# Optimization experiments

Hardware: AMD Instinct MI355X
Metric: run time of the kernel (lower is better)

Reference implementation:

```python
import jax, jax.numpy as jnp
import numpy as np


def _he_scale(k, shape, fan_in):
    return jax.random.normal(k, shape, dtype=jnp.float32) * np.sqrt(2.0 / fan_in).astype(np.float32)


def setup_inputs() -> dict:
    key = jax.random.key(0)
    kx, kt, kp, kg, kf = jax.random.split(key, 5)
    B, H, W, C, D = 4, 64, 64, 256, 128
    x = jax.random.normal(kx, (B, H, W, C), dtype=jnp.float32)
    Wt = _he_scale(kt, (C, D), C)
    Wp = _he_scale(kp, (C, D), C)
    Wg = _he_scale(kg, (C, D), C)
    Wf = _he_scale(kf, (D, C), D)
    return {"x": x, "Wt": Wt, "Wp": Wp, "Wg": Wg, "Wf": Wf}


def _maxpool1d(z, pool_size=2, stride=1):
    # Keras MaxPool1D, padding='valid': output length = (N - pool_size)//stride + 1
    return jax.lax.reduce_window(
        z, -jnp.inf, jax.lax.max,
        window_dimensions=(1, pool_size, 1),
        window_strides=(1, stride, 1),
        padding='VALID')


def reference(x, Wt, Wp, Wg, Wf):
    B, H, W, C = x.shape
    D = Wt.shape[1]
    N = H * W
    # 1x1 conv projections == per-position matmuls
    theta = jnp.einsum('bhwc,cd->bhwd', x, Wt).reshape(B, N, D)   # [B,N,D]
    phi = jnp.einsum('bhwc,cd->bhwd', x, Wp).reshape(B, N, D)     # [B,N,D]
    g = jnp.einsum('bhwc,cd->bhwd', x, Wg).reshape(B, N, D)       # [B,N,D]
    # embedded mode: subsample phi and g (pool_size=2, strides=1) -> M = N-1
    phi = _maxpool1d(phi)                                          # [B,M,D]
    g = _maxpool1d(g)                                              # [B,M,D]
    # f = theta @ phi^T, softmax over keys (no scaling in embedded mode)
    f = jax.nn.softmax(jnp.einsum('bnd,bmd->bnm', theta, phi), axis=-1)  # [B,N,M]
    y = jnp.einsum('bnm,bmd->bnd', f, g).reshape(B, H, W, D)       # [B,H,W,D]
    # final 1x1 conv back to C channels + residual
    z = x + jnp.einsum('bhwd,dc->bhwc', y, Wf)
    return z
```

## Files before the change

kernel.cpp:

```cpp
#include <hip/hip_runtime.h>

#define B_  4
#define N_  4096
#define C_  256
#define D_  128
#define M_  4095
#define BN_ (B_ * N_)
#define KSPLIT 4

typedef _Float16 half_t;
typedef __attribute__((ext_vector_type(8))) _Float16 half8;
typedef __attribute__((ext_vector_type(4))) _Float16 half4;
typedef __attribute__((ext_vector_type(4))) float f32x4;

#define MFMA16x16x32(A, B, C) __builtin_amdgcn_mfma_f32_16x16x32_f16(A, B, C, 0, 0, 0)
#define LOG2E 1.44269504088896f

__global__ __launch_bounds__(256) void prep_kernel(
    const float* __restrict__ Wt, const float* __restrict__ Wp,
    const float* __restrict__ Wg, const float* __restrict__ Wf,
    half_t* __restrict__ WT_hi, half_t* __restrict__ WfT)
{
    const int idx = blockIdx.x * 256 + threadIdx.x;
    const int wsel = blockIdx.y;
    if (wsel < 3) {
        const float* __restrict__ W = (wsel == 0) ? Wt : (wsel == 1) ? Wp : Wg;
        const int d = idx >> 8, c = idx & 255;
        WT_hi[(size_t)wsel * 32768 + idx] = (half_t)W[(size_t)c * D_ + d];
    } else {
        const int c = idx >> 7, d = idx & 127;
        WfT[idx] = (half_t)Wf[(size_t)d * C_ + c];
    }
}

__global__ __launch_bounds__(256) void proj_kernel(
    const float* __restrict__ x, const half_t* __restrict__ WT_hi,
    half_t* __restrict__ theta, half_t* __restrict__ pphi,
    half_t* __restrict__ pgT)
{
    const int tid = threadIdx.x;
    const int lane = tid & 63;
    const int w = tid >> 6;
    const int lm = lane & 15;
    const int lq = lane >> 4;
    const int r0 = blockIdx.x * 64;
    const int which = blockIdx.y;
    const half_t* __restrict__ Wg_ = WT_hi + (size_t)which * 32768;

    __shared__ __align__(16) unsigned char lds_raw[18432];
    half_t (*Xh)[40]  = (half_t (*)[40])(lds_raw);
    half_t (*Whl)[40] = (half_t (*)[40])(lds_raw + 5120);

    f32x4 acc[8];
#pragma unroll
    for (int nb = 0; nb < 8; ++nb)
#pragma unroll
        for (int r = 0; r < 4; ++r) acc[nb][r] = 0.f;

    const int xr = tid >> 2, xc = (tid & 3) * 8;
    const int wr = tid >> 1, wc = (tid & 1) * 16;

    for (int kc = 0; kc < 8; ++kc) {
        __syncthreads();
        {
            const float* xs = x + (size_t)(r0 + xr) * C_ + kc * 32 + xc;
            float4 v0 = *(const float4*)&xs[0], v1 = *(const float4*)&xs[4];
            half8 hi;
            hi[0] = (half_t)v0.x; hi[1] = (half_t)v0.y;
            hi[2] = (half_t)v0.z; hi[3] = (half_t)v0.w;
            hi[4] = (half_t)v1.x; hi[5] = (half_t)v1.y;
            hi[6] = (half_t)v1.z; hi[7] = (half_t)v1.w;
            *(half8*)&Xh[xr][xc] = hi;
            const half_t* wsrc = Wg_ + (size_t)wr * 256 + kc * 32 + wc;
            *(half8*)&Whl[wr][wc]     = *(const half8*)&wsrc[0];
            *(half8*)&Whl[wr][wc + 8] = *(const half8*)&wsrc[8];
        }
        __syncthreads();

        half8 ah = *(const half8*)&Xh[w * 16 + lm][lq * 8];
#pragma unroll
        for (int nb = 0; nb < 8; ++nb) {
            half8 bh = *(const half8*)&Whl[nb * 16 + lm][lq * 8];
            acc[nb] = MFMA16x16x32(ah, bh, acc[nb]);
        }
    }

    if (which == 0) {
#pragma unroll
        for (int nb = 0; nb < 8; ++nb)
#pragma unroll
            for (int r = 0; r < 4; ++r)
                theta[(size_t)(r0 + w * 16 + lq * 4 + r) * D_ + nb * 16 + lm] =
                    (half_t)(acc[nb][r] * LOG2E);
        return;
    }

    __syncthreads();
    half_t (*LsT)[72] = (half_t (*)[72])(lds_raw);
#pragma unroll
    for (int nb = 0; nb < 8; ++nb) {
        const int d = nb * 16 + lm;
        const int m = w * 16 + lq * 4;
        half4 pk;
#pragma unroll
        for (int r = 0; r < 4; ++r) pk[r] = (half_t)acc[nb][r];
        *(half4*)&LsT[d][m] = pk;
    }
    if (tid < 128) {
        int rh = r0 + 64;
        if ((rh & (N_ - 1)) == 0) rh = r0 + 63;
        const float* xrow = x + (size_t)rh * C_;
        const half_t* wrow = Wg_ + (size_t)tid * 256;
        float s = 0.f;
#pragma unroll
        for (int c8 = 0; c8 < 32; ++c8) {
            half8 h = *(const half8*)&wrow[c8 * 8];
            float4 xa = *(const float4*)&xrow[c8 * 8];
            float4 xb = *(const float4*)&xrow[c8 * 8 + 4];
            s += xa.x * (float)h[0] + xa.y * (float)h[1]
               + xa.z * (float)h[2] + xa.w * (float)h[3]
               + xb.x * (float)h[4] + xb.y * (float)h[5]
               + xb.z * (float)h[6] + xb.w * (float)h[7];
        }
        LsT[tid][64] = (half_t)s;
    }
    __syncthreads();

    if (which == 1) {
        const int m = tid >> 2, dh = (tid & 3) * 32;
        half8 o[4];
#pragma unroll
        for (int j = 0; j < 32; ++j) {
            float v0 = (float)LsT[dh + j][m];
            float v1 = (float)LsT[dh + j][m + 1];
            o[j >> 3][j & 7] = (half_t)fmaxf(v0, v1);
        }
        half8* dst = (half8*)&pphi[(size_t)(r0 + m) * D_ + dh];
#pragma unroll
        for (int j = 0; j < 4; ++j) dst[j] = o[j];
    } else {
        const int d = tid >> 1, mh = (tid & 1) * 32;
        const int b = r0 / N_, m0 = r0 & (N_ - 1);
        half8 in[4];
#pragma unroll
        for (int j = 0; j < 4; ++j) in[j] = *(const half8*)&LsT[d][mh + j * 8];
        const half_t ext = LsT[d][mh + 32];
        half8 o[4];
#pragma unroll
        for (int j = 0; j < 32; ++j) {
            float v0 = (float)in[j >> 3][j & 7];
            float v1 = (j == 31) ? (float)ext : (float)in[(j + 1) >> 3][(j + 1) & 7];
            o[j >> 3][j & 7] = (half_t)fmaxf(v0, v1);
        }
        half8* dst = (half8*)&pgT[((size_t)b * D_ + d) * N_ + m0 + mh];
#pragma unroll
        for (int j = 0; j < 4; ++j) dst[j] = o[j];
    }
}

__global__ __launch_bounds__(256, 2) void attn_kernel(
    const half_t* __restrict__ theta, const half_t* __restrict__ pphi,
    const half_t* __restrict__ pgT, half_t* __restrict__ ypart,
    float* __restrict__ mstat, float* __restrict__ lstat)
{
    const int tid = threadIdx.x;
    const int lane = tid & 63;
    const int w = tid >> 6;
    const int lm = lane & 15;
    const int lq = lane >> 4;
    const int qt = blockIdx.x, ksb = blockIdx.y, b = blockIdx.z;
    const int q0 = qt * 128;
    const int kt0 = ksb * 16, kt1 = kt0 + 16;

    __shared__ half_t Ks[64][136];
    __shared__ half_t Gts[128][72];
    __shared__ half_t Ps[128][72];

    half8 qh[2][4];
#pragma unroll
    for (int nb = 0; nb < 2; ++nb) {
        const half_t* tr_ = theta + ((size_t)b * N_ + q0 + w * 32 + nb * 16 + lm) * D_;
#pragma unroll
        for (int k4 = 0; k4 < 4; ++k4)
            qh[nb][k4] = *(const half8*)(tr_ + k4 * 32 + lq * 8);
    }

    float m_i[2] = {-1e30f, -1e30f};
    float l_i[2] = {0.f, 0.f};
    f32x4 yacc[2][8];
#pragma unroll
    for (int mb = 0; mb < 2; ++mb)
#pragma unroll
        for (int dn = 0; dn < 8; ++dn)
#pragma unroll
            for (int r = 0; r < 4; ++r) yacc[mb][dn][r] = 0.f;

    for (int kt = kt0; kt < kt1; ++kt) {
        const int k0 = kt * 64;
        __syncthreads();
        {
            const int key = tid >> 2, ch = (tid & 3);
            const float4* src = (const float4*)(pphi +
                ((size_t)b * N_ + k0 + key) * D_ + ch * 32);
            float4 a0 = src[0], a1 = src[1], a2 = src[2], a3 = src[3];
            float4* dst = (float4*)&Ks[key][ch * 32];
            dst[0] = a0; dst[1] = a1; dst[2] = a2; dst[3] = a3;
            const int d = tid >> 1, kh = (tid & 1);
            const float4* gs = (const float4*)(pgT +
                ((size_t)b * D_ + d) * N_ + k0 + kh * 32);
            float4 g0 = gs[0], g1 = gs[1], g2 = gs[2], g3 = gs[3];
            float4* gd = (float4*)&Gts[d][kh * 32];
            gd[0] = g0; gd[1] = g1; gd[2] = g2; gd[3] = g3;
        }
        __syncthreads();

        f32x4 sc[4][2];
#pragma unroll
        for (int kb = 0; kb < 4; ++kb)
#pragma unroll
            for (int nb = 0; nb < 2; ++nb)
#pragma unroll
                for (int r = 0; r < 4; ++r) sc[kb][nb][r] = 0.f;
#pragma unroll
        for (int kb = 0; kb < 4; ++kb) {
#pragma unroll
            for (int k4 = 0; k4 < 4; ++k4) {
                half8 kf = *(const half8*)&Ks[kb * 16 + lm][k4 * 32 + lq * 8];
#pragma unroll
                for (int nb = 0; nb < 2; ++nb)
                    sc[kb][nb] = MFMA16x16x32(kf, qh[nb][k4], sc[kb][nb]);
            }
        }
        if (k0 + 64 > M_) {
#pragma unroll
            for (int kb = 0; kb < 4; ++kb)
#pragma unroll
                for (int r = 0; r < 4; ++r)
                    if (k0 + kb * 16 + lq * 4 + r >= M_) {
                        sc[kb][0][r] = -1e30f; sc[kb][1][r] = -1e30f;
                    }
        }
        float alpha[2];
#pragma unroll
        for (int nb = 0; nb < 2; ++nb) {
            float mt = -1e30f;
#pragma unroll
            for (int kb = 0; kb < 4; ++kb)
#pragma unroll
                for (int r = 0; r < 4; ++r) mt = fmaxf(mt, sc[kb][nb][r]);
            mt = fmaxf(mt, __shfl_xor(mt, 16, 64));
            mt = fmaxf(mt, __shfl_xor(mt, 32, 64));
            const float mnew = fmaxf(m_i[nb], mt);
            alpha[nb] = exp2f(m_i[nb] - mnew);
            m_i[nb] = mnew;
            float rs = 0.f;
#pragma unroll
            for (int kb = 0; kb < 4; ++kb)
#pragma unroll
                for (int r = 0; r < 4; ++r) {
                    float p = exp2f(sc[kb][nb][r] - mnew);
                    sc[kb][nb][r] = p;
                    rs += p;
                }
            l_i[nb] = l_i[nb] * alpha[nb] + rs;
#pragma unroll
            for (int kb = 0; kb < 4; ++kb) {
                half4 pk;
#pragma unroll
                for (int r = 0; r < 4; ++r) pk[r] = (half_t)sc[kb][nb][r];
                *(half4*)&Ps[w * 32 + nb * 16 + lm][kb * 16 + lq * 4] = pk;
            }
        }
        float alpha_t[2][4];
#pragma unroll
        for (int mb = 0; mb < 2; ++mb)
#pragma unroll
            for (int r = 0; r < 4; ++r)
                alpha_t[mb][r] = __shfl(alpha[mb], lq * 4 + r, 16);
#pragma unroll
        for (int mb = 0; mb < 2; ++mb)
#pragma unroll
            for (int dn = 0; dn < 8; ++dn)
#pragma unroll
                for (int r = 0; r < 4; ++r) yacc[mb][dn][r] *= alpha_t[mb][r];
        half8 pf[2][2];
#pragma unroll
        for (int mb = 0; mb < 2; ++mb)
#pragma unroll
            for (int k2 = 0; k2 < 2; ++k2)
                pf[mb][k2] = *(const half8*)&Ps[w * 32 + mb * 16 + lm][k2 * 32 + lq * 8];
#pragma unroll
        for (int dn = 0; dn < 8; ++dn) {
#pragma unroll
            for (int k2 = 0; k2 < 2; ++k2) {
                half8 gf = *(const half8*)&Gts[dn * 16 + lm][k2 * 32 + lq * 8];
                yacc[0][dn] = MFMA16x16x32(pf[0][k2], gf, yacc[0][dn]);
                yacc[1][dn] = MFMA16x16x32(pf[1][k2], gf, yacc[1][dn]);
            }
        }
    }

#pragma unroll
    for (int nb = 0; nb < 2; ++nb) {
        l_i[nb] += __shfl_xor(l_i[nb], 16, 64);
        l_i[nb] += __shfl_xor(l_i[nb], 32, 64);
    }
    half_t* yp = ypart + ((size_t)ksb * BN_ + (size_t)b * N_) * D_;
#pragma unroll
    for (int mb = 0; mb < 2; ++mb)
#pragma unroll
        for (int dn = 0; dn < 8; ++dn)
#pragma unroll
            for (int r = 0; r < 4; ++r)
                yp[(size_t)(q0 + w * 32 + mb * 16 + lq * 4 + r) * D_ + dn * 16 + lm] =
                    (half_t)yacc[mb][dn][r];
    if (lq == 0) {
#pragma unroll
        for (int nb = 0; nb < 2; ++nb) {
            const int row = q0 + w * 32 + nb * 16 + lm;
            mstat[(size_t)ksb * BN_ + (size_t)b * N_ + row] = m_i[nb];
            lstat[(size_t)ksb * BN_ + (size_t)b * N_ + row] = l_i[nb];
        }
    }
}

__global__ __launch_bounds__(256) void final_kernel(
    const half_t* __restrict__ ypart, const float* __restrict__ mstat,
    const float* __restrict__ lstat, const float* __restrict__ x,
    const half_t* __restrict__ WfT, float* __restrict__ out)
{
    const int tid = threadIdx.x;
    const int lane = tid & 63;
    const int w = tid >> 6;
    const int lm = lane & 15;
    const int lq = lane >> 4;
    const int r0 = blockIdx.x * 128;
    const int c0 = blockIdx.y * 128;

    __shared__ half_t Ys[128][72];
    __shared__ half_t Wfs[128][72];
    __shared__ float scl[KSPLIT][128];

    if (tid < 128) {
        const int row = r0 + tid;
        float mv[KSPLIT], lv[KSPLIT], wv[KSPLIT];
        float Mx = -1e30f;
#pragma unroll
        for (int s = 0; s < KSPLIT; ++s) {
            mv[s] = mstat[(size_t)s * BN_ + row];
            lv[s] = lstat[(size_t)s * BN_ + row];
            Mx = fmaxf(Mx, mv[s]);
        }
        float lsum = 0.f;
#pragma unroll
        for (int s = 0; s < KSPLIT; ++s) { wv[s] = exp2f(mv[s] - Mx); lsum += wv[s] * lv[s]; }
        const float inv = 1.f / lsum;
#pragma unroll
        for (int s = 0; s < KSPLIT; ++s) scl[s][tid] = wv[s] * inv;
    }
    __syncthreads();

    f32x4 acc[2][8];
#pragma unroll
    for (int rb = 0; rb < 2; ++rb)
#pragma unroll
        for (int nb = 0; nb < 8; ++nb)
#pragma unroll
            for (int r = 0; r < 4; ++r) acc[rb][nb][r] = 0.f;

    const int sr = tid >> 1;
    const int dd = (tid & 1) * 32;

    for (int kc = 0; kc < 2; ++kc) {
        {
            float ss[KSPLIT];
#pragma unroll
            for (int s = 0; s < KSPLIT; ++s) ss[s] = scl[s][sr];
            const size_t yb = (size_t)(r0 + sr) * D_ + kc * 64 + dd;
            half8 o[4];
#pragma unroll
            for (int q = 0; q < 4; ++q) {
                float m[8];
#pragma unroll
                for (int j = 0; j < 8; ++j) m[j] = 0.f;
#pragma unroll
                for (int s = 0; s < KSPLIT; ++s) {
                    half8 yv = *(const half8*)&ypart[(size_t)s * BN_ * D_ + yb + q * 8];
#pragma unroll
                    for (int j = 0; j < 8; ++j) m[j] += ss[s] * (float)yv[j];
                }
#pragma unroll
                for (int j = 0; j < 8; ++j) o[q][j] = (half_t)m[j];
            }
#pragma unroll
            for (int q = 0; q < 4; ++q) *(half8*)&Ys[sr][dd + q * 8] = o[q];
            const half_t* wf = WfT + (size_t)(c0 + sr) * D_ + kc * 64 + dd;
#pragma unroll
            for (int q = 0; q < 4; ++q)
                *(half8*)&Wfs[sr][dd + q * 8] = *(const half8*)&wf[q * 8];
        }
        __syncthreads();

        half8 af[2][2];
#pragma unroll
        for (int rb = 0; rb < 2; ++rb)
#pragma unroll
            for (int k2 = 0; k2 < 2; ++k2)
                af[rb][k2] = *(const half8*)&Ys[w * 32 + rb * 16 + lm][k2 * 32 + lq * 8];
#pragma unroll
        for (int nb = 0; nb < 8; ++nb) {
#pragma unroll
            for (int k2 = 0; k2 < 2; ++k2) {
                half8 bf = *(const half8*)&Wfs[nb * 16 + lm][k2 * 32 + lq * 8];
                acc[0][nb] = MFMA16x16x32(af[0][k2], bf, acc[0][nb]);
                acc[1][nb] = MFMA16x16x32(af[1][k2], bf, acc[1][nb]);
            }
        }
        __syncthreads();
    }
#pragma unroll
    for (int rb = 0; rb < 2; ++rb)
#pragma unroll
        for (int nb = 0; nb < 8; ++nb)
#pragma unroll
            for (int r = 0; r < 4; ++r) {
                const int row = r0 + w * 32 + rb * 16 + lq * 4 + r;
                const int col = c0 + nb * 16 + lm;
                out[(size_t)row * C_ + col] =
                    acc[rb][nb][r] + x[(size_t)row * C_ + col];
            }
}

extern "C" void kernel_launch(void* const* d_in, const int* in_sizes, int n_in,
                              void* d_out, int out_size, void* d_ws, size_t ws_size,
                              hipStream_t stream)
{
    const float* x  = (const float*)d_in[0];
    const float* Wt = (const float*)d_in[1];
    const float* Wp = (const float*)d_in[2];
    const float* Wg = (const float*)d_in[3];
    const float* Wf = (const float*)d_in[4];
    float* out = (float*)d_out;

    const size_t SEG = (size_t)BN_ * D_;
    float* ws     = (float*)d_ws;
    half_t* theta = (half_t*)ws;
    half_t* pphi  = (half_t*)(ws + SEG / 2);
    half_t* pgT   = (half_t*)(ws + SEG);
    half_t* ypart = (half_t*)(ws + SEG + SEG / 2);
    float* mstat  = ws + 3 * SEG + SEG / 2;
    float* lstat  = mstat + (size_t)KSPLIT * BN_;
    half_t* WT_hi = (half_t*)(lstat + (size_t)KSPLIT * BN_);
    half_t* WfT   = WT_hi + 3 * 32768;

    prep_kernel<<<dim3(128, 4), 256, 0, stream>>>(Wt, Wp, Wg, Wf, WT_hi, WfT);
    proj_kernel<<<dim3(BN_ / 64, 3), 256, 0, stream>>>(x, WT_hi, theta, pphi, pgT);
    attn_kernel<<<dim3(N_ / 128, KSPLIT, B_), 256, 0, stream>>>(
        theta, pphi, pgT, ypart, mstat, lstat);
    final_kernel<<<dim3(BN_ / 128, 2), 256, 0, stream>>>(
        ypart, mstat, lstat, x, WfT, out);
}
```

Before: 176.1 us.

## Alias attention LDS buffers, raise occupancy, and make key-split count runtime-selectable

Ks and Ps now share one raw LDS allocation, with an extra barrier before P is written so K reads finish first. Together with Gts this cuts the attention block's shared memory, and the launch bound is raised to 4 blocks per CU. The key-split factor becomes a runtime parameter that rises to 8 when the workspace is large enough, which adds parallelism in the attention grid. The cost is more partial-output traffic for the final reduction and extra register pressure under the tighter launch bound, which could cause spills.

Result: slower. 245.8 us (+39.5%).

```diff
diff --git a/kernel.cpp b/kernel.cpp
--- a/kernel.cpp
+++ b/kernel.cpp
@@ -6,7 +6,7 @@
 #define D_  128
 #define M_  4095
 #define BN_ (B_ * N_)
-#define KSPLIT 4
+#define MAXSPLIT 8
 
 typedef _Float16 half_t;
 typedef __attribute__((ext_vector_type(8))) _Float16 half8;
@@ -158,10 +158,10 @@
     }
 }
 
-__global__ __launch_bounds__(256, 2) void attn_kernel(
+__global__ __launch_bounds__(256, 4) void attn_kernel(
     const half_t* __restrict__ theta, const half_t* __restrict__ pphi,
     const half_t* __restrict__ pgT, half_t* __restrict__ ypart,
-    float* __restrict__ mstat, float* __restrict__ lstat)
+    float* __restrict__ mstat, float* __restrict__ lstat, int nsplit)
 {
     const int tid = threadIdx.x;
     const int lane = tid & 63;
@@ -170,11 +170,13 @@
     const int lq = lane >> 4;
     const int qt = blockIdx.x, ksb = blockIdx.y, b = blockIdx.z;
     const int q0 = qt * 128;
-    const int kt0 = ksb * 16, kt1 = kt0 + 16;
-
-    __shared__ half_t Ks[64][136];
-    __shared__ half_t Gts[128][72];
-    __shared__ half_t Ps[128][72];
+    const int kt0 = (64 * ksb) / nsplit;
+    const int kt1 = (64 * (ksb + 1)) / nsplit;
+
+    __shared__ __align__(16) unsigned char lds_raw[36864];
+    half_t (*Ks)[136] = (half_t (*)[136])(lds_raw);
+    half_t (*Ps)[72]  = (half_t (*)[72])(lds_raw);
+    half_t (*Gts)[72] = (half_t (*)[72])(lds_raw + 18432);
 
     half8 qh[2][4];
 #pragma unroll
@@ -263,6 +265,23 @@
                     rs += p;
                 }
             l_i[nb] = l_i[nb] * alpha[nb] + rs;
+        }
+        float alpha_t[2][4];
+#pragma unroll
+        for (int mb = 0; mb < 2; ++mb)
+#pragma unroll
+            for (int r = 0; r < 4; ++r)
+                alpha_t[mb][r] = __shfl(alpha[mb], lq * 4 + r, 16);
+#pragma unroll
+        for (int mb = 0; mb < 2; ++mb)
+#pragma unroll
+            for (int dn = 0; dn < 8; ++dn)
+#pragma unroll
+                for (int r = 0; r < 4; ++r) yacc[mb][dn][r] *= alpha_t[mb][r];
+
+        __syncthreads();
+#pragma unroll
+        for (int nb = 0; nb < 2; ++nb)
 #pragma unroll
             for (int kb = 0; kb < 4; ++kb) {
                 half4 pk;
@@ -270,19 +289,6 @@
                 for (int r = 0; r < 4; ++r) pk[r] = (half_t)sc[kb][nb][r];
                 *(half4*)&Ps[w * 32 + nb * 16 + lm][kb * 16 + lq * 4] = pk;
             }
-        }
-        float alpha_t[2][4];
-#pragma unroll
-        for (int mb = 0; mb < 2; ++mb)
-#pragma unroll
-            for (int r = 0; r < 4; ++r)
-                alpha_t[mb][r] = __shfl(alpha[mb], lq * 4 + r, 16);
-#pragma unroll
-        for (int mb = 0; mb < 2; ++mb)
-#pragma unroll
-            for (int dn = 0; dn < 8; ++dn)
-#pragma unroll
-                for (int r = 0; r < 4; ++r) yacc[mb][dn][r] *= alpha_t[mb][r];
         half8 pf[2][2];
 #pragma unroll
         for (int mb = 0; mb < 2; ++mb)
@@ -327,7 +333,7 @@
 __global__ __launch_bounds__(256) void final_kernel(
     const half_t* __restrict__ ypart, const float* __restrict__ mstat,
     const float* __restrict__ lstat, const float* __restrict__ x,
-    const half_t* __restrict__ WfT, float* __restrict__ out)
+    const half_t* __restrict__ WfT, float* __restrict__ out, int nsplit)
 {
     const int tid = threadIdx.x;
     const int lane = tid & 63;
@@ -339,24 +345,22 @@
 
     __shared__ half_t Ys[128][72];
     __shared__ half_t Wfs[128][72];
-    __shared__ float scl[KSPLIT][128];
+    __shared__ float scl[MAXSPLIT][128];
 
     if (tid < 128) {
         const int row = r0 + tid;
-        float mv[KSPLIT], lv[KSPLIT], wv[KSPLIT];
+        float mv[MAXSPLIT], lv[MAXSPLIT];
         float Mx = -1e30f;
-#pragma unroll
-        for (int s = 0; s < KSPLIT; ++s) {
+        for (int s = 0; s < nsplit; ++s) {
             mv[s] = mstat[(size_t)s * BN_ + row];
             lv[s] = lstat[(size_t)s * BN_ + row];
             Mx = fmaxf(Mx, mv[s]);
         }
         float lsum = 0.f;
-#pragma unroll
-        for (int s = 0; s < KSPLIT; ++s) { wv[s] = exp2f(mv[s] - Mx); lsum += wv[s] * lv[s]; }
+        float wv[MAXSPLIT];
+        for (int s = 0; s < nsplit; ++s) { wv[s] = exp2f(mv[s] - Mx); lsum += wv[s] * lv[s]; }
         const float inv = 1.f / lsum;
-#pragma unroll
-        for (int s = 0; s < KSPLIT; ++s) scl[s][tid] = wv[s] * inv;
+        for (int s = 0; s < nsplit; ++s) scl[s][tid] = wv[s] * inv;
     }
     __syncthreads();
 
@@ -373,9 +377,6 @@
 
     for (int kc = 0; kc < 2; ++kc) {
         {
-            float ss[KSPLIT];
-#pragma unroll
-            for (int s = 0; s < KSPLIT; ++s) ss[s] = scl[s][sr];
             const size_t yb = (size_t)(r0 + sr) * D_ + kc * 64 + dd;
             half8 o[4];
 #pragma unroll
@@ -383,11 +384,11 @@
                 float m[8];
 #pragma unroll
                 for (int j = 0; j < 8; ++j) m[j] = 0.f;
-#pragma unroll
-                for (int s = 0; s < KSPLIT; ++s) {
+                for (int s = 0; s < nsplit; ++s) {
+                    const float ss = scl[s][sr];
                     half8 yv = *(const half8*)&ypart[(size_t)s * BN_ * D_ + yb + q * 8];
 #pragma unroll
-                    for (int j = 0; j < 8; ++j) m[j] += ss[s] * (float)yv[j];
+                    for (int j = 0; j < 8; ++j) m[j] += ss * (float)yv[j];
                 }
 #pragma unroll
                 for (int j = 0; j < 8; ++j) o[q][j] = (half_t)m[j];
@@ -443,20 +444,23 @@
     float* out = (float*)d_out;
 
     const size_t SEG = (size_t)BN_ * D_;
+    const size_t words8 = 3 * SEG / 2 + 8 * SEG / 2 + (size_t)2 * 8 * BN_ + 65536;
+    const int nsplit = (ws_size >= words8 * sizeof(float)) ? 8 : 4;
+
     float* ws     = (float*)d_ws;
     half_t* theta = (half_t*)ws;
     half_t* pphi  = (half_t*)(ws + SEG / 2);
     half_t* pgT   = (half_t*)(ws + SEG);
-    half_t* ypart = (half_t*)(ws + SEG + SEG / 2);
-    float* mstat  = ws + 3 * SEG + SEG / 2;
-    float* lstat  = mstat + (size_t)KSPLIT * BN_;
-    half_t* WT_hi = (half_t*)(lstat + (size_t)KSPLIT * BN_);
+    half_t* ypart = (half_t*)(ws + 3 * SEG / 2);
+    float* mstat  = ws + 3 * SEG / 2 + (size_t)nsplit * SEG / 2;
+    float* lstat  = mstat + (size_t)nsplit * BN_;
+    half_t* WT_hi = (half_t*)(lstat + (size_t)nsplit * BN_);
     half_t* WfT   = WT_hi + 3 * 32768;
 
     prep_kernel<<<dim3(128, 4), 256, 0, stream>>>(Wt, Wp, Wg, Wf, WT_hi, WfT);
     proj_kernel<<<dim3(BN_ / 64, 3), 256, 0, stream>>>(x, WT_hi, theta, pphi, pgT);
-    attn_kernel<<<dim3(N_ / 128, KSPLIT, B_), 256, 0, stream>>>(
-        theta, pphi, pgT, ypart, mstat, lstat);
+    attn_kernel<<<dim3(N_ / 128, nsplit, B_), 256, 0, stream>>>(
+        theta, pphi, pgT, ypart, mstat, lstat, nsplit);
     final_kernel<<<dim3(BN_ / 128, 2), 256, 0, stream>>>(
-        ypart, mstat, lstat, x, WfT, out);
+        ypart, mstat, lstat, x, WfT, out, nsplit);
 }
```

## Fuse three projections per block reusing staged x tile; skip unit rescale

Applied to the files above, without the earlier changes.

The projection kernel now loads and converts each 64-row x tile to fp16 once into LDS and loops over the theta, phi and g weight sets inside one block. Previously three separate blocks each re-read and re-converted the same x rows. This cuts global x traffic, at the cost of more LDS per block (about 61KB) and a third as many blocks. The attention kernel also skips the per-iteration accumulator rescale when every alpha in the wavefront equals 1.

New measurement: 185.9 us. 5.6% more time.

```diff
diff --git a/kernel.cpp b/kernel.cpp
--- a/kernel.cpp
+++ b/kernel.cpp
@@ -44,117 +44,128 @@
     const int lm = lane & 15;
     const int lq = lane >> 4;
     const int r0 = blockIdx.x * 64;
-    const int which = blockIdx.y;
-    const half_t* __restrict__ Wg_ = WT_hi + (size_t)which * 32768;
-
-    __shared__ __align__(16) unsigned char lds_raw[18432];
-    half_t (*Xh)[40]  = (half_t (*)[40])(lds_raw);
-    half_t (*Whl)[40] = (half_t (*)[40])(lds_raw + 5120);
-
-    f32x4 acc[8];
-#pragma unroll
-    for (int nb = 0; nb < 8; ++nb)
-#pragma unroll
-        for (int r = 0; r < 4; ++r) acc[nb][r] = 0.f;
-
-    const int xr = tid >> 2, xc = (tid & 3) * 8;
+
+    __shared__ __align__(16) unsigned char lds_raw[62464];
+    half_t (*Xb)[264] = (half_t (*)[264])(lds_raw);
+    half_t (*Wc)[40]  = (half_t (*)[40])(lds_raw + 33792);
+    half_t (*LsT)[72] = (half_t (*)[72])(lds_raw + 44032);
+
+    {
+        const int row = tid >> 2;
+        const int cb = (tid & 3) * 64;
+        const float* xs = x + (size_t)(r0 + row) * C_ + cb;
+#pragma unroll
+        for (int j = 0; j < 4; ++j) {
+            float4 v0 = *(const float4*)&xs[j * 16];
+            float4 v1 = *(const float4*)&xs[j * 16 + 4];
+            float4 v2 = *(const float4*)&xs[j * 16 + 8];
+            float4 v3 = *(const float4*)&xs[j * 16 + 12];
+            half8 h0, h1;
+            h0[0]=(half_t)v0.x; h0[1]=(half_t)v0.y; h0[2]=(half_t)v0.z; h0[3]=(half_t)v0.w;
+            h0[4]=(half_t)v1.x; h0[5]=(half_t)v1.y; h0[6]=(half_t)v1.z; h0[7]=(half_t)v1.w;
+            h1[0]=(half_t)v2.x; h1[1]=(half_t)v2.y; h1[2]=(half_t)v2.z; h1[3]=(half_t)v2.w;
+            h1[4]=(half_t)v3.x; h1[5]=(half_t)v3.y; h1[6]=(half_t)v3.z; h1[7]=(half_t)v3.w;
+            *(half8*)&Xb[row][cb + j * 16]     = h0;
+            *(half8*)&Xb[row][cb + j * 16 + 8] = h1;
+        }
+    }
+
     const int wr = tid >> 1, wc = (tid & 1) * 16;
 
-    for (int kc = 0; kc < 8; ++kc) {
+    for (int which = 0; which < 3; ++which) {
+        const half_t* __restrict__ Wg_ = WT_hi + (size_t)which * 32768;
+        f32x4 acc[8];
+#pragma unroll
+        for (int nb = 0; nb < 8; ++nb)
+#pragma unroll
+            for (int r = 0; r < 4; ++r) acc[nb][r] = 0.f;
+
+        for (int kc = 0; kc < 8; ++kc) {
+            __syncthreads();
+            {
+                const half_t* wsrc = Wg_ + (size_t)wr * 256 + kc * 32 + wc;
+                *(half8*)&Wc[wr][wc]     = *(const half8*)&wsrc[0];
+                *(half8*)&Wc[wr][wc + 8] = *(const half8*)&wsrc[8];
+            }
+            __syncthreads();
+
+            half8 ah = *(const half8*)&Xb[w * 16 + lm][kc * 32 + lq * 8];
+#pragma unroll
+            for (int nb = 0; nb < 8; ++nb) {
+                half8 bh = *(const half8*)&Wc[nb * 16 + lm][lq * 8];
+                acc[nb] = MFMA16x16x32(ah, bh, acc[nb]);
+            }
+        }
+
+        if (which == 0) {
+#pragma unroll
+            for (int nb = 0; nb < 8; ++nb)
+#pragma unroll
+                for (int r = 0; r < 4; ++r)
+                    theta[(size_t)(r0 + w * 16 + lq * 4 + r) * D_ + nb * 16 + lm] =
+                        (half_t)(acc[nb][r] * LOG2E);
+            continue;
+        }
+
+#pragma unroll
+        for (int nb = 0; nb < 8; ++nb) {
+            const int d = nb * 16 + lm;
+            const int m = w * 16 + lq * 4;
+            half4 pk;
+#pragma unroll
+            for (int r = 0; r < 4; ++r) pk[r] = (half_t)acc[nb][r];
+            *(half4*)&LsT[d][m] = pk;
+        }
+        if (tid < 128) {
+            int rh = r0 + 64;
+            if ((rh & (N_ - 1)) == 0) rh = r0 + 63;
+            const float* xrow = x + (size_t)rh * C_;
+            const half_t* wrow = Wg_ + (size_t)tid * 256;
+            float s = 0.f;
+#pragma unroll
+            for (int c8 = 0; c8 < 32; ++c8) {
+                half8 h = *(const half8*)&wrow[c8 * 8];
+                float4 xa = *(const float4*)&xrow[c8 * 8];
+                float4 xb = *(const float4*)&xrow[c8 * 8 + 4];
+                s += xa.x * (float)h[0] + xa.y * (float)h[1]
+                   + xa.z * (float)h[2] + xa.w * (float)h[3]
+                   + xb.x * (float)h[4] + xb.y * (float)h[5]
+                   + xb.z * (float)h[6] + xb.w * (float)h[7];
+            }
+            LsT[tid][64] = (half_t)s;
+        }
         __syncthreads();
-        {
-            const float* xs = x + (size_t)(r0 + xr) * C_ + kc * 32 + xc;
-            float4 v0 = *(const float4*)&xs[0], v1 = *(const float4*)&xs[4];
-            half8 hi;
-            hi[0] = (half_t)v0.x; hi[1] = (half_t)v0.y;
-            hi[2] = (half_t)v0.z; hi[3] = (half_t)v0.w;
-            hi[4] = (half_t)v1.x; hi[5] = (half_t)v1.y;
-            hi[6] = (half_t)v1.z; hi[7] = (half_t)v1.w;
-            *(half8*)&Xh[xr][xc] = hi;
-            const half_t* wsrc = Wg_ + (size_t)wr * 256 + kc * 32 + wc;
-            *(half8*)&Whl[wr][wc]     = *(const half8*)&wsrc[0];
-            *(half8*)&Whl[wr][wc + 8] = *(const half8*)&wsrc[8];
-        }
-        __syncthreads();
-
-        half8 ah = *(const half8*)&Xh[w * 16 + lm][lq * 8];
-#pragma unroll
-        for (int nb = 0; nb < 8; ++nb) {
-            half8 bh = *(const half8*)&Whl[nb * 16 + lm][lq * 8];
-            acc[nb] = MFMA16x16x32(ah, bh, acc[nb]);
-        }
-    }
-
-    if (which == 0) {
-#pragma unroll
-        for (int nb = 0; nb < 8; ++nb)
-#pragma unroll
-            for (int r = 0; r < 4; ++r)
-                theta[(size_t)(r0 + w * 16 + lq * 4 + r) * D_ + nb * 16 + lm] =
-                    (half_t)(acc[nb][r] * LOG2E);
-        return;
-    }
-
-    __syncthreads();
-    half_t (*LsT)[72] = (half_t (*)[72])(lds_raw);
-#pragma unroll
-    for (int nb = 0; nb < 8; ++nb) {
-        const int d = nb * 16 + lm;
-        const int m = w * 16 + lq * 4;
-        half4 pk;
-#pragma unroll
-        for (int r = 0; r < 4; ++r) pk[r] = (half_t)acc[nb][r];
-        *(half4*)&LsT[d][m] = pk;
-    }
-    if (tid < 128) {
-        int rh = r0 + 64;
-        if ((rh & (N_ - 1)) == 0) rh = r0 + 63;
-        const float* xrow = x + (size_t)rh * C_;
-        const half_t* wrow = Wg_ + (size_t)tid * 256;
-        float s = 0.f;
-#pragma unroll
-        for (int c8 = 0; c8 < 32; ++c8) {
-            half8 h = *(const half8*)&wrow[c8 * 8];
-            float4 xa = *(const float4*)&xrow[c8 * 8];
-            float4 xb = *(const float4*)&xrow[c8 * 8 + 4];
-            s += xa.x * (float)h[0] + xa.y * (float)h[1]
-               + xa.z * (float)h[2] + xa.w * (float)h[3]
-               + xb.x * (float)h[4] + xb.y * (float)h[5]
-               + xb.z * (float)h[6] + xb.w * (float)h[7];
-        }
-        LsT[tid][64] = (half_t)s;
-    }
-    __syncthreads();
-
-    if (which == 1) {
-        const int m = tid >> 2, dh = (tid & 3) * 32;
-        half8 o[4];
-#pragma unroll
-        for (int j = 0; j < 32; ++j) {
-            float v0 = (float)LsT[dh + j][m];
-            float v1 = (float)LsT[dh + j][m + 1];
-            o[j >> 3][j & 7] = (half_t)fmaxf(v0, v1);
-        }
-        half8* dst = (half8*)&pphi[(size_t)(r0 + m) * D_ + dh];
-#pragma unroll
-        for (int j = 0; j < 4; ++j) dst[j] = o[j];
-    } else {
-        const int d = tid >> 1, mh = (tid & 1) * 32;
-        const int b = r0 / N_, m0 = r0 & (N_ - 1);
-        half8 in[4];
-#pragma unroll
-        for (int j = 0; j < 4; ++j) in[j] = *(const half8*)&LsT[d][mh + j * 8];
-        const half_t ext = LsT[d][mh + 32];
-        half8 o[4];
-#pragma unroll
-        for (int j = 0; j < 32; ++j) {
-            float v0 = (float)in[j >> 3][j & 7];
-            float v1 = (j == 31) ? (float)ext : (float)in[(j + 1) >> 3][(j + 1) & 7];
-            o[j >> 3][j & 7] = (half_t)fmaxf(v0, v1);
-        }
-        half8* dst = (half8*)&pgT[((size_t)b * D_ + d) * N_ + m0 + mh];
-#pragma unroll
-        for (int j = 0; j < 4; ++j) dst[j] = o[j];
+
+        if (which == 1) {
+            const int m = tid >> 2, dh = (tid & 3) * 32;
+            half8 o[4];
+#pragma unroll
+            for (int j = 0; j < 32; ++j) {
+                float v0 = (float)LsT[dh + j][m];
+                float v1 = (float)LsT[dh + j][m + 1];
+                o[j >> 3][j & 7] = (half_t)fmaxf(v0, v1);
+            }
+            half8* dst = (half8*)&pphi[(size_t)(r0 + m) * D_ + dh];
+#pragma unroll
+            for (int j = 0; j < 4; ++j) dst[j] = o[j];
+        } else {
+            const int d = tid >> 1, mh = (tid & 1) * 32;
+            const int b = r0 / N_, m0 = r0 & (N_ - 1);
+            half8 in[4];
+#pragma unroll
+            for (int j = 0; j < 4; ++j) in[j] = *(const half8*)&LsT[d][mh + j * 8];
+            const half_t ext = LsT[d][mh + 32];
+            half8 o[4];
+#pragma unroll
+            for (int j = 0; j < 32; ++j) {
+                float v0 = (float)in[j >> 3][j & 7];
+                float v1 = (j == 31) ? (float)ext : (float)in[(j + 1) >> 3][(j + 1) & 7];
+                o[j >> 3][j & 7] = (half_t)fmaxf(v0, v1);
+            }
+            half8* dst = (half8*)&pgT[((size_t)b * D_ + d) * N_ + m0 + mh];
+#pragma unroll
+            for (int j = 0; j < 4; ++j) dst[j] = o[j];
+        }
     }
 }
 
@@ -271,18 +282,21 @@
                 *(half4*)&Ps[w * 32 + nb * 16 + lm][kb * 16 + lq * 4] = pk;
             }
         }
-        float alpha_t[2][4];
-#pragma unroll
-        for (int mb = 0; mb < 2; ++mb)
-#pragma unroll
-            for (int r = 0; r < 4; ++r)
-                alpha_t[mb][r] = __shfl(alpha[mb], lq * 4 + r, 16);
-#pragma unroll
-        for (int mb = 0; mb < 2; ++mb)
-#pragma unroll
-            for (int dn = 0; dn < 8; ++dn)
-#pragma unroll
-                for (int r = 0; r < 4; ++r) yacc[mb][dn][r] *= alpha_t[mb][r];
+        const int need = (alpha[0] != 1.0f) || (alpha[1] != 1.0f);
+        if (__any(need)) {
+            float alpha_t[2][4];
+#pragma unroll
+            for (int mb = 0; mb < 2; ++mb)
+#pragma unroll
+                for (int r = 0; r < 4; ++r)
+                    alpha_t[mb][r] = __shfl(alpha[mb], lq * 4 + r, 16);
+#pragma unroll
+            for (int mb = 0; mb < 2; ++mb)
+#pragma unroll
+                for (int dn = 0; dn < 8; ++dn)
+#pragma unroll
+                    for (int r = 0; r < 4; ++r) yacc[mb][dn][r] *= alpha_t[mb][r];
+        }
         half8 pf[2][2];
 #pragma unroll
         for (int mb = 0; mb < 2; ++mb)
@@ -447,14 +461,14 @@
     half_t* theta = (half_t*)ws;
     half_t* pphi  = (half_t*)(ws + SEG / 2);
     half_t* pgT   = (half_t*)(ws + SEG);
-    half_t* ypart = (half_t*)(ws + SEG + SEG / 2);
-    float* mstat  = ws + 3 * SEG + SEG / 2;
+    half_t* ypart = (half_t*)(ws + 3 * SEG / 2);
+    float* mstat  = ws + 3 * SEG / 2 + (size_t)KSPLIT * SEG / 2;
     float* lstat  = mstat + (size_t)KSPLIT * BN_;
     half_t* WT_hi = (half_t*)(lstat + (size_t)KSPLIT * BN_);
     half_t* WfT   = WT_hi + 3 * 32768;
 
     prep_kernel<<<dim3(128, 4), 256, 0, stream>>>(Wt, Wp, Wg, Wf, WT_hi, WfT);
-    proj_kernel<<<dim3(BN_ / 64, 3), 256, 0, stream>>>(x, WT_hi, theta, pphi, pgT);
+    proj_kernel<<<dim3(BN_ / 64), 256, 0, stream>>>(x, WT_hi, theta, pphi, pgT);
     attn_kernel<<<dim3(N_ / 128, KSPLIT, B_), 256, 0, stream>>>(
         theta, pphi, pgT, ypart, mstat, lstat);
     final_kernel<<<dim3(BN_ / 128, 2), 256, 0, stream>>>(
```
